# Kernel tuning notes

Measured on AMD Instinct MI355X. Metric: run time of the kernel, lower is better.

Reference implementation:

```python
import jax, jax.numpy as jnp
import numpy as np
import math

PC_MIN_X, PC_MIN_Y = 0.0, -40.0
VOXEL = 0.05
STRIDE = 8
PE_CH = 16
NEG_SLOPE = 0.01
BN_EPS = 1e-5


def _grid_points():
    # get_pseudo_points: centers of stride-8 BEV cells
    xs = np.arange(0.2, 70.4, 0.4, dtype=np.float32)    # 176
    ys = np.arange(-39.8, 40.2, 0.4, dtype=np.float32)  # 200
    gx, gy = np.meshgrid(xs, ys)                        # (200, 176)
    return jnp.asarray(np.stack([gx, gy], -1).reshape(-1, 2))  # [P, 2]


def _pe3d(D, H, W):
    ch = PE_CH
    div = jnp.exp(jnp.arange(0, ch, 2, dtype=jnp.float32) * (-math.log(10000.0) / ch))
    def enc(n):
        t = jnp.arange(n, dtype=jnp.float32)[:, None] * div[None, :]
        return jnp.concatenate([jnp.sin(t), jnp.cos(t)], axis=-1)  # [n, ch]
    pex = jnp.broadcast_to(enc(D)[:, None, None, :], (D, H, W, ch))
    pey = jnp.broadcast_to(enc(H)[None, :, None, :], (D, H, W, ch))
    pez = jnp.broadcast_to(enc(W)[None, None, :, :], (D, H, W, ch))
    return jnp.concatenate([pex, pey, pez], axis=-1).transpose(3, 0, 1, 2)  # [3*ch, D, H, W]


def _bn_lrelu(h, g, b):
    # eval-mode BatchNorm3d with running_mean=0, running_var=1, then LeakyReLU(0.01)
    h = h * (g / np.sqrt(1.0 + BN_EPS))[None, :, None, None, None] + b[None, :, None, None, None]
    return jnp.where(h >= 0, h, NEG_SLOPE * h)


def _dvf(x, w1, b1, g1, be1, w2, b2, g2, be2, w3, b3):
    N, C, D, H, W = x.shape
    pe = _pe3d(D, H, W)  # [48, D, H, W]
    feats = jnp.concatenate([x, jnp.broadcast_to(pe[None], (N,) + pe.shape)], axis=1)
    h = jnp.einsum('ncdhw,oc->nodhw', feats, w1) + b1[None, :, None, None, None]
    h = _bn_lrelu(h, g1, be1)
    h = jnp.einsum('ncdhw,oc->nodhw', h, w2) + b2[None, :, None, None, None]
    h = _bn_lrelu(h, g2, be2)
    logits = jnp.einsum('ncdhw,oc->nodhw', h, w3) + b3[None, :, None, None, None]  # [N,1,D,H,W]
    wts = jax.nn.softmax(logits, axis=2)  # softmax over depth D
    return (x * wts).reshape(N, C * D, H, W)


def _bilinear(im, x, y):
    # im: (H, W, C), x/y: (P,)  -- faithful to bilinear_interpolate_torch
    H, W = im.shape[0], im.shape[1]
    xf = jnp.floor(x).astype(jnp.int32)
    yf = jnp.floor(y).astype(jnp.int32)
    x0 = jnp.clip(xf, 0, W - 1)
    x1 = jnp.clip(xf + 1, 0, W - 1)
    y0 = jnp.clip(yf, 0, H - 1)
    y1 = jnp.clip(yf + 1, 0, H - 1)
    Ia, Ib, Ic, Id = im[y0, x0], im[y1, x0], im[y0, x1], im[y1, x1]
    x0f, x1f = x0.astype(x.dtype), x1.astype(x.dtype)
    y0f, y1f = y0.astype(y.dtype), y1.astype(y.dtype)
    wa = (x1f - x) * (y1f - y)
    wb = (x1f - x) * (y - y0f)
    wc = (x - x0f) * (y1f - y)
    wd = (x - x0f) * (y - y0f)
    return Ia * wa[:, None] + Ib * wb[:, None] + Ic * wc[:, None] + Id * wd[:, None]


def _rot(p, theta):
    c, s = jnp.cos(theta), jnp.sin(theta)
    return jnp.stack([p[:, 0] * c - p[:, 1] * s, p[:, 0] * s + p[:, 1] * c], axis=-1)


def _bev_align_one(feat, th_prev, th_cur, grid):
    # feat: [C', H, W]; X_TRANS modeled as z-rotation: fwd(current) then inverse(previous)
    Hh, Ww = feat.shape[1], feat.shape[2]
    p = _rot(grid, th_cur)
    p = _rot(p, -th_prev)
    xi = (p[:, 0] - PC_MIN_X) / VOXEL / STRIDE
    yi = (p[:, 1] - PC_MIN_Y) / VOXEL / STRIDE
    out = _bilinear(feat.transpose(1, 2, 0), xi, yi)  # [P, C']
    return out.reshape(Hh, Ww, -1).transpose(2, 0, 1)


def setup_inputs() -> dict:
    key = jax.random.key(0)
    ks = jax.random.split(key, 16)
    N, C, D, H, W = 4, 64, 2, 200, 176
    IN1 = PE_CH * 3 + C  # 112
    inp = {
        'x0': jax.random.normal(ks[0], (N, C, D, H, W), jnp.float32),
        'x1': jax.random.normal(ks[1], (N, C, D, H, W), jnp.float32),
        'transform_param': jax.random.normal(ks[2], (N, 2), jnp.float32) * 0.3,
        'w1': jax.random.normal(ks[3], (C, IN1), jnp.float32) * 0.05,
        'b1': jax.random.normal(ks[4], (C,), jnp.float32) * 0.05,
        'g1': jax.random.uniform(ks[5], (C,), jnp.float32, 0.5, 1.5),
        'be1': jax.random.normal(ks[6], (C,), jnp.float32) * 0.05,
        'w2': jax.random.normal(ks[7], (C // 2, C), jnp.float32) * 0.05,
        'b2': jax.random.normal(ks[8], (C // 2,), jnp.float32) * 0.05,
        'g2': jax.random.uniform(ks[9], (C // 2,), jnp.float32, 0.5, 1.5),
        'be2': jax.random.normal(ks[10], (C // 2,), jnp.float32) * 0.05,
        'w3': jax.random.normal(ks[11], (1, C // 2), jnp.float32) * 0.05,
        'b3': jax.random.normal(ks[12], (1,), jnp.float32) * 0.05,
    }
    return inp


def reference(x0, x1, transform_param, w1, b1, g1, be1, w2, b2, g2, be2, w3, b3):
    mlp = (w1, b1, g1, be1, w2, b2, g2, be2, w3, b3)
    f0 = _dvf(x0, *mlp)  # rot 0: [N, C*D, H, W]
    f1 = _dvf(x1, *mlp)  # rot 1
    grid = _grid_points()
    aligned = jax.vmap(lambda f, tp: _bev_align_one(f, tp[0], tp[1], grid))(f1, transform_param)
    return jnp.maximum(f0, aligned)  # ALIGN_METHOD='max' over stacked feats
```

## Files before the change

### kernel.cpp

```cpp
#include <hip/hip_runtime.h>
#include <hip/hip_bf16.h>
#include <cmath>

#define HW   35200
#define CD   128

typedef short bf16x8 __attribute__((ext_vector_type(8)));
typedef float f32x4  __attribute__((ext_vector_type(4)));
typedef unsigned int u32;

union Frag { unsigned u[4]; bf16x8 v; };

#define GLD16(srcp, dstp) \
  __builtin_amdgcn_global_load_lds((const __attribute__((address_space(1))) u32*)(const void*)(srcp), \
                                   (__attribute__((address_space(3))) u32*)(void*)(dstp), 16, 0, 0)

#define OFF_W1B   0
#define OFF_W2B   3072
#define OFF_TD    4096
#define OFF_B2F   4224
#define OFF_W3F   4256
#define OFF_PE    4288
#define OFF_F0B   567488
#define OFF_F1B   9578688

__device__ __forceinline__ float lrelu(float v) { return v >= 0.f ? v : 0.01f * v; }
__device__ __forceinline__ unsigned short f2bf(float f) {
  union { __hip_bfloat16 h; unsigned short u; } c;
  c.h = __float2bfloat16(f);
  return c.u;
}
__device__ __forceinline__ unsigned pack2bf(float lo, float hi) {
  union { __hip_bfloat162 h2; unsigned u; } c;
  c.h2 = __float22bfloat162_rn(float2{lo, hi});
  return c.u;
}
__device__ __forceinline__ float bflo(unsigned u) { return __uint_as_float(u << 16); }
__device__ __forceinline__ float bfhi(unsigned u) { return __uint_as_float(u & 0xffff0000u); }

__global__ void setup_kernel(const float* __restrict__ w1, const float* __restrict__ b1,
                             const float* __restrict__ g1, const float* __restrict__ be1,
                             const float* __restrict__ w2, const float* __restrict__ b2,
                             const float* __restrict__ g2, const float* __restrict__ be2,
                             const float* __restrict__ w3, const float* __restrict__ b3,
                             float* __restrict__ ws) {
  const float RS = rsqrtf(1.0f + 1e-5f);
  unsigned short* w1b = (unsigned short*)(ws + OFF_W1B);
  unsigned short* w2b = (unsigned short*)(ws + OFF_W2B);
  unsigned short* pe  = (unsigned short*)(ws + OFF_PE);
  int i = blockIdx.x * blockDim.x + threadIdx.x;
  if (i < 6144) {
    int e = i & 7, l = (i >> 3) & 63, nt = (i >> 9) & 3, kh = i >> 11;
    int n = nt * 16 + (l & 15);
    int k = kh * 32 + (l >> 4) * 8 + e;
    int col = (kh < 2) ? k : (80 + (k - 64));
    w1b[i] = f2bf(w1[n * 112 + col] * (g1[n] * RS));
    return;
  }
  i -= 6144;
  if (i < 2048) {
    int e = i & 7, l = (i >> 3) & 63, nt = (i >> 9) & 1, kh = i >> 10;
    int n = nt * 16 + (l & 15);
    int k = kh * 32 + (l >> 4) * 8 + e;
    w2b[i] = f2bf(w2[n * 64 + k] * (g2[n] * RS));
    return;
  }
  i -= 2048;
  if (i < 128) {
    int d = i >> 6, o = i & 63;
    float a = 0.f;
    for (int j = 0; j < 8; ++j) {
      float dv = expf((float)(2 * j) * (-0.5756462732485115f));
      float t  = (float)d * dv;
      a += w1[o * 112 + 64 + j] * sinf(t) + w1[o * 112 + 72 + j] * cosf(t);
    }
    ws[OFF_TD + d * 64 + o] = (g1[o] * RS) * (b1[o] + a) + be1[o];
    return;
  }
  i -= 128;
  if (i < 32) { ws[OFF_B2F + i] = b2[i] * (g2[i] * RS) + be2[i]; return; }
  i -= 32;
  if (i < 32) { ws[OFF_W3F + i] = w3[i]; return; }
  i -= 32;
  if (i < 563200) {
    int hw = i >> 4, j = i & 15;
    int h = hw / 176, w = hw - h * 176;
    int jj = j & 7;
    float dv = expf((float)(2 * jj) * (-0.5756462732485115f));
    if (j < 8) {
      float t = (float)h * dv;
      pe[hw * 32 + jj]      = f2bf(sinf(t));
      pe[hw * 32 + 8 + jj]  = f2bf(cosf(t));
    } else {
      float t = (float)w * dv;
      pe[hw * 32 + 16 + jj] = f2bf(sinf(t));
      pe[hw * 32 + 24 + jj] = f2bf(cosf(t));
    }
  }
}

__global__ __launch_bounds__(256)
void mlp_kernel(const float* __restrict__ x0, const float* __restrict__ x1,
                const float* __restrict__ wtab,
                unsigned short* __restrict__ f0b, unsigned short* __restrict__ f1b) {
  __shared__ alignas(16) unsigned char Sm[32768];

  const int t    = threadIdx.x;
  const int lane = t & 63;
  const int wv   = __builtin_amdgcn_readfirstlane(t >> 6);
  const int g    = lane >> 4;
  const int li   = lane & 15;
  const int n    = blockIdx.y;
  const int inp  = blockIdx.z;
  const int hw0w = blockIdx.x * 64 + wv * 16;
  const int px   = hw0w + li;
  const float* xn = (inp ? x1 : x0) + (size_t)n * CD * HW;
  unsigned short* dst = inp ? f1b : f0b;
  const unsigned short* w1bu = (const unsigned short*)(wtab + OFF_W1B);
  const unsigned short* w2bu = (const unsigned short*)(wtab + OFF_W2B);
  const unsigned short* peg  = (const unsigned short*)(wtab + OFF_PE);
  unsigned char* Wb = Sm + wv * 8192;

  const uint4 pev = *(const uint4*)(peg + (size_t)px * 32 + g * 8);

#pragma unroll
  for (int j = 0; j < 8; ++j) {
    const int plane = 2 * (8 * j + (lane >> 3)) + ((lane & 1) ^ (j & 1));
    const int q     = (((lane >> 1) & 3) - j) & 3;
    GLD16(xn + (size_t)plane * HW + hw0w + q * 4, Wb + j * 1024);
  }
  asm volatile("s_waitcnt vmcnt(0)" ::: "memory");
  __builtin_amdgcn_sched_barrier(0);

  const float* Wf = (const float*)Wb;
  const int qbase = (((li >> 2) + g) & 3) * 8 + (li & 3);
  Frag xb[2][2];
#pragma unroll
  for (int d = 0; d < 2; ++d) {
    const int dof = (d ^ (g & 1)) * 4;
#pragma unroll
    for (int kh = 0; kh < 2; ++kh)
#pragma unroll
      for (int q2 = 0; q2 < 4; ++q2) {
        const float v0 = Wf[(32 * kh + 8 * g + 2 * q2 + 0) * 32 + qbase + dof];
        const float v1 = Wf[(32 * kh + 8 * g + 2 * q2 + 1) * 32 + qbase + dof];
        xb[d][kh].u[q2] = pack2bf(v0, v1);
      }
  }
  Frag pf;
  pf.u[0] = pev.x; pf.u[1] = pev.y; pf.u[2] = pev.z; pf.u[3] = pev.w;

  f32x4 acc[2][4];
#pragma unroll
  for (int d = 0; d < 2; ++d)
#pragma unroll
    for (int nt = 0; nt < 4; ++nt) {
      const float tdv = wtab[OFF_TD + d * 64 + nt * 16 + li];
      acc[d][nt] = (f32x4){tdv, tdv, tdv, tdv};
    }
#pragma unroll
  for (int kh = 0; kh < 2; ++kh)
#pragma unroll
    for (int nt = 0; nt < 4; ++nt) {
      const bf16x8 b = *(const bf16x8*)&w1bu[(unsigned)((kh * 4 + nt) * 64 + lane) * 8];
      acc[0][nt] = __builtin_amdgcn_mfma_f32_16x16x32_bf16(xb[0][kh].v, b, acc[0][nt], 0, 0, 0);
      acc[1][nt] = __builtin_amdgcn_mfma_f32_16x16x32_bf16(xb[1][kh].v, b, acc[1][nt], 0, 0, 0);
    }
#pragma unroll
  for (int nt = 0; nt < 4; ++nt) {
    const bf16x8 b = *(const bf16x8*)&w1bu[(unsigned)((8 + nt) * 64 + lane) * 8];
    acc[0][nt] = __builtin_amdgcn_mfma_f32_16x16x32_bf16(pf.v, b, acc[0][nt], 0, 0, 0);
    acc[1][nt] = __builtin_amdgcn_mfma_f32_16x16x32_bf16(pf.v, b, acc[1][nt], 0, 0, 0);
  }
  __builtin_amdgcn_sched_barrier(0);

  unsigned short* Hsw = (unsigned short*)Wb;
#pragma unroll
  for (int d = 0; d < 2; ++d)
#pragma unroll
    for (int nt = 0; nt < 4; ++nt)
#pragma unroll
      for (int r = 0; r < 4; ++r) {
        const int o   = nt * 16 + li;
        const int row = d * 16 + g * 4 + r;
        Hsw[(unsigned)(((o >> 3) * 32 + row) * 8 + (o & 7))] = f2bf(lrelu(acc[d][nt][r]));
      }

  f32x4 acc2[2][2];
#pragma unroll
  for (int nt = 0; nt < 2; ++nt) {
    const float bv = wtab[OFF_B2F + nt * 16 + li];
    acc2[0][nt] = (f32x4){bv, bv, bv, bv};
    acc2[1][nt] = acc2[0][nt];
  }
#pragma unroll
  for (int kh = 0; kh < 2; ++kh) {
    const bf16x8 a0 = *(const bf16x8*)&Hsw[(unsigned)(((kh * 4 + g) * 32 + 0 * 16 + li) * 8)];
    const bf16x8 a1 = *(const bf16x8*)&Hsw[(unsigned)(((kh * 4 + g) * 32 + 1 * 16 + li) * 8)];
#pragma unroll
    for (int nt = 0; nt < 2; ++nt) {
      const bf16x8 b = *(const bf16x8*)&w2bu[(unsigned)((kh * 2 + nt) * 64 + lane) * 8];
      acc2[0][nt] = __builtin_amdgcn_mfma_f32_16x16x32_bf16(a0, b, acc2[0][nt], 0, 0, 0);
      acc2[1][nt] = __builtin_amdgcn_mfma_f32_16x16x32_bf16(a1, b, acc2[1][nt], 0, 0, 0);
    }
  }

  const float w3a = wtab[OFF_W3F + li];
  const float w3b = wtab[OFF_W3F + 16 + li];
  float wt0[4], wt1[4];
#pragma unroll
  for (int r = 0; r < 4; ++r) {
    float p0 = w3a * lrelu(acc2[0][0][r]) + w3b * lrelu(acc2[0][1][r]);
    float p1 = w3a * lrelu(acc2[1][0][r]) + w3b * lrelu(acc2[1][1][r]);
    p0 += __shfl_xor(p0, 1); p0 += __shfl_xor(p0, 2);
    p0 += __shfl_xor(p0, 4); p0 += __shfl_xor(p0, 8);
    p1 += __shfl_xor(p1, 1); p1 += __shfl_xor(p1, 2);
    p1 += __shfl_xor(p1, 4); p1 += __shfl_xor(p1, 8);
    wt0[r] = 1.f / (1.f + expf(p1 - p0));
    wt1[r] = 1.f / (1.f + expf(p0 - p1));
  }

  const int src = (li >> 2) << 4;
  float a0 = __shfl(wt0[0], src), b0 = __shfl(wt1[0], src);
  float a1 = __shfl(wt0[1], src), b1v = __shfl(wt1[1], src);
  float a2 = __shfl(wt0[2], src), b2v = __shfl(wt1[2], src);
  float a3 = __shfl(wt0[3], src), b3v = __shfl(wt1[3], src);
  const int rs = li & 3;
  const float w0  = (rs == 0) ? a0 : (rs == 1) ? a1 : (rs == 2) ? a2 : a3;
  const float w1v = (rs == 0) ? b0 : (rs == 1) ? b1v : (rs == 2) ? b2v : b3v;

#pragma unroll
  for (int kh = 0; kh < 2; ++kh)
#pragma unroll
    for (int j = 0; j < 4; ++j) {
      const int k = kh * 16 + g * 4 + j;
      const unsigned ua = xb[0][kh].u[j];
      const unsigned ub = xb[1][kh].u[j];
      uint2 pk;
      pk.x = pack2bf(bflo(ua) * w0, bflo(ub) * w1v);
      pk.y = pack2bf(bfhi(ua) * w0, bfhi(ub) * w1v);
      *(uint2*)&dst[(((size_t)n * 32 + k) * HW + px) * 4] = pk;
    }
}

__global__ __launch_bounds__(256)
void gather_max_kernel(const unsigned short* __restrict__ f0b,
                       const unsigned short* __restrict__ f1b,
                       const float* __restrict__ tp,
                       float* __restrict__ out) {
  const int orig = blockIdx.x;
  const int xcd = orig & 7, idx = orig >> 3;
  const int tile = (xcd < 6 ? xcd * 69 : 6 * 69 + (xcd - 6) * 68) + idx;

  const int tix = threadIdx.x;
  const int px  = tix & 63;
  const int q   = tix >> 6;
  const int n   = blockIdx.y;
  const int hw  = tile * 64 + px;
  const int h   = hw / 176;
  const int w   = hw - h * 176;

  const float thp = tp[n * 2 + 0], thc = tp[n * 2 + 1];
  const float gx = 0.2f + 0.4f * (float)w;
  const float gy = -39.8f + 0.4f * (float)h;
  const float c1 = cosf(thc),  s1v = sinf(thc);
  const float p1x = gx * c1 - gy * s1v;
  const float p1y = gx * s1v + gy * c1;
  const float c2 = cosf(-thp), s2v = sinf(-thp);
  const float p2x = p1x * c2 - p1y * s2v;
  const float p2y = p1x * s2v + p1y * c2;
  const float xi = p2x / 0.05f / 8.f;
  const float yi = (p2y - (-40.f)) / 0.05f / 8.f;

  const float xf = floorf(xi), yf = floorf(yi);
  const int x0i = (int)xf, y0i = (int)yf;
  const int x0c = min(max(x0i,     0), 175);
  const int x1c = min(max(x0i + 1, 0), 175);
  const int y0c = min(max(y0i,     0), 199);
  const int y1c = min(max(y0i + 1, 0), 199);
  const float x0f = (float)x0c, x1f = (float)x1c;
  const float y0f = (float)y0c, y1f = (float)y1c;
  const float wa = (x1f - xi) * (y1f - yi);
  const float wb = (x1f - xi) * (yi - y0f);
  const float wc = (xi - x0f) * (y1f - yi);
  const float wd = (xi - x0f) * (yi - y0f);
  const int ta = y0c * 176 + x0c, tb = y1c * 176 + x0c;
  const int tc = y0c * 176 + x1c, td = y1c * 176 + x1c;

#pragma unroll
  for (int i = 0; i < 8; ++i) {
    const int k = q * 8 + i;
    const int cd0 = k * 4;
    const unsigned short* fp1 = f1b + ((size_t)n * 32 + k) * HW * 4;
    const uint2 Ia = *(const uint2*)(fp1 + (size_t)ta * 4);
    const uint2 Ib = *(const uint2*)(fp1 + (size_t)tb * 4);
    const uint2 Ic = *(const uint2*)(fp1 + (size_t)tc * 4);
    const uint2 Id = *(const uint2*)(fp1 + (size_t)td * 4);
    float4 sv;
    sv.x = bflo(Ia.x) * wa + bflo(Ib.x) * wb + bflo(Ic.x) * wc + bflo(Id.x) * wd;
    sv.y = bfhi(Ia.x) * wa + bfhi(Ib.x) * wb + bfhi(Ic.x) * wc + bfhi(Id.x) * wd;
    sv.z = bflo(Ia.y) * wa + bflo(Ib.y) * wb + bflo(Ic.y) * wc + bflo(Id.y) * wd;
    sv.w = bfhi(Ia.y) * wa + bfhi(Ib.y) * wb + bfhi(Ic.y) * wc + bfhi(Id.y) * wd;

    const uint2 F0 = *(const uint2*)(f0b + (((size_t)n * 32 + k) * HW + hw) * 4);

    float* op = out + ((size_t)n * CD + cd0) * HW + hw;
    op[0]              = fmaxf(bflo(F0.x), sv.x);
    op[HW]             = fmaxf(bfhi(F0.x), sv.y);
    op[2 * (size_t)HW] = fmaxf(bflo(F0.y), sv.z);
    op[3 * (size_t)HW] = fmaxf(bfhi(F0.y), sv.w);
  }
}

extern "C" void kernel_launch(void* const* d_in, const int* in_sizes, int n_in,
                              void* d_out, int out_size, void* d_ws, size_t ws_size,
                              hipStream_t stream) {
  const float* x0  = (const float*)d_in[0];
  const float* x1  = (const float*)d_in[1];
  const float* tp  = (const float*)d_in[2];
  const float* w1  = (const float*)d_in[3];
  const float* b1  = (const float*)d_in[4];
  const float* g1  = (const float*)d_in[5];
  const float* be1 = (const float*)d_in[6];
  const float* w2  = (const float*)d_in[7];
  const float* b2  = (const float*)d_in[8];
  const float* g2  = (const float*)d_in[9];
  const float* be2 = (const float*)d_in[10];
  const float* w3  = (const float*)d_in[11];
  const float* b3  = (const float*)d_in[12];
  float* ws = (float*)d_ws;
  unsigned short* f0b = (unsigned short*)(ws + OFF_F0B);
  unsigned short* f1b = (unsigned short*)(ws + OFF_F1B);

  setup_kernel<<<2233, 256, 0, stream>>>(w1, b1, g1, be1, w2, b2, g2, be2, w3, b3, ws);

  dim3 g1d(550, 4, 2);
  mlp_kernel<<<g1d, 256, 0, stream>>>(x0, x1, ws, f0b, f1b);

  dim3 g2d(550, 4);
  gather_max_kernel<<<g2d, 256, 0, stream>>>(f0b, f1b, tp, (float*)d_out);
}
```

Baseline: 85.48 us.

## Double-buffer async LDS loads across five pixel tiles per wave in MLP kernel

```diff
diff --git a/kernel.cpp b/kernel.cpp
--- a/kernel.cpp
+++ b/kernel.cpp
@@ -99,148 +99,169 @@
   }
 }
 
-__global__ __launch_bounds__(256)
+__global__ __launch_bounds__(128)
 void mlp_kernel(const float* __restrict__ x0, const float* __restrict__ x1,
                 const float* __restrict__ wtab,
                 unsigned short* __restrict__ f0b, unsigned short* __restrict__ f1b) {
-  __shared__ alignas(16) unsigned char Sm[32768];
-
-  const int t    = threadIdx.x;
-  const int lane = t & 63;
-  const int wv   = __builtin_amdgcn_readfirstlane(t >> 6);
+  __shared__ alignas(16) unsigned char Sm[40960];
+
+  const int t0   = threadIdx.x;
+  const int lane = t0 & 63;
+  const int wv   = __builtin_amdgcn_readfirstlane(t0 >> 6);
   const int g    = lane >> 4;
   const int li   = lane & 15;
   const int n    = blockIdx.y;
   const int inp  = blockIdx.z;
-  const int hw0w = blockIdx.x * 64 + wv * 16;
-  const int px   = hw0w + li;
+  const int base = blockIdx.x * 160 + wv * 16;
   const float* xn = (inp ? x1 : x0) + (size_t)n * CD * HW;
   unsigned short* dst = inp ? f1b : f0b;
   const unsigned short* w1bu = (const unsigned short*)(wtab + OFF_W1B);
   const unsigned short* w2bu = (const unsigned short*)(wtab + OFF_W2B);
   const unsigned short* peg  = (const unsigned short*)(wtab + OFF_PE);
-  unsigned char* Wb = Sm + wv * 8192;
-
-  const uint4 pev = *(const uint4*)(peg + (size_t)px * 32 + g * 8);
-
-#pragma unroll
-  for (int j = 0; j < 8; ++j) {
-    const int plane = 2 * (8 * j + (lane >> 3)) + ((lane & 1) ^ (j & 1));
-    const int q     = (((lane >> 1) & 3) - j) & 3;
-    GLD16(xn + (size_t)plane * HW + hw0w + q * 4, Wb + j * 1024);
-  }
-  asm volatile("s_waitcnt vmcnt(0)" ::: "memory");
-  __builtin_amdgcn_sched_barrier(0);
-
-  const float* Wf = (const float*)Wb;
-  const int qbase = (((li >> 2) + g) & 3) * 8 + (li & 3);
-  Frag xb[2][2];
-#pragma unroll
-  for (int d = 0; d < 2; ++d) {
-    const int dof = (d ^ (g & 1)) * 4;
-#pragma unroll
-    for (int kh = 0; kh < 2; ++kh)
-#pragma unroll
-      for (int q2 = 0; q2 < 4; ++q2) {
-        const float v0 = Wf[(32 * kh + 8 * g + 2 * q2 + 0) * 32 + qbase + dof];
-        const float v1 = Wf[(32 * kh + 8 * g + 2 * q2 + 1) * 32 + qbase + dof];
-        xb[d][kh].u[q2] = pack2bf(v0, v1);
-      }
-  }
-  Frag pf;
-  pf.u[0] = pev.x; pf.u[1] = pev.y; pf.u[2] = pev.z; pf.u[3] = pev.w;
-
-  f32x4 acc[2][4];
-#pragma unroll
-  for (int d = 0; d < 2; ++d)
-#pragma unroll
-    for (int nt = 0; nt < 4; ++nt) {
-      const float tdv = wtab[OFF_TD + d * 64 + nt * 16 + li];
-      acc[d][nt] = (f32x4){tdv, tdv, tdv, tdv};
-    }
-#pragma unroll
-  for (int kh = 0; kh < 2; ++kh)
-#pragma unroll
-    for (int nt = 0; nt < 4; ++nt) {
-      const bf16x8 b = *(const bf16x8*)&w1bu[(unsigned)((kh * 4 + nt) * 64 + lane) * 8];
-      acc[0][nt] = __builtin_amdgcn_mfma_f32_16x16x32_bf16(xb[0][kh].v, b, acc[0][nt], 0, 0, 0);
-      acc[1][nt] = __builtin_amdgcn_mfma_f32_16x16x32_bf16(xb[1][kh].v, b, acc[1][nt], 0, 0, 0);
-    }
-#pragma unroll
-  for (int nt = 0; nt < 4; ++nt) {
-    const bf16x8 b = *(const bf16x8*)&w1bu[(unsigned)((8 + nt) * 64 + lane) * 8];
-    acc[0][nt] = __builtin_amdgcn_mfma_f32_16x16x32_bf16(pf.v, b, acc[0][nt], 0, 0, 0);
-    acc[1][nt] = __builtin_amdgcn_mfma_f32_16x16x32_bf16(pf.v, b, acc[1][nt], 0, 0, 0);
-  }
-  __builtin_amdgcn_sched_barrier(0);
-
-  unsigned short* Hsw = (unsigned short*)Wb;
-#pragma unroll
-  for (int d = 0; d < 2; ++d)
-#pragma unroll
-    for (int nt = 0; nt < 4; ++nt)
-#pragma unroll
-      for (int r = 0; r < 4; ++r) {
-        const int o   = nt * 16 + li;
-        const int row = d * 16 + g * 4 + r;
-        Hsw[(unsigned)(((o >> 3) * 32 + row) * 8 + (o & 7))] = f2bf(lrelu(acc[d][nt][r]));
-      }
-
-  f32x4 acc2[2][2];
-#pragma unroll
-  for (int nt = 0; nt < 2; ++nt) {
-    const float bv = wtab[OFF_B2F + nt * 16 + li];
-    acc2[0][nt] = (f32x4){bv, bv, bv, bv};
-    acc2[1][nt] = acc2[0][nt];
-  }
-#pragma unroll
-  for (int kh = 0; kh < 2; ++kh) {
-    const bf16x8 a0 = *(const bf16x8*)&Hsw[(unsigned)(((kh * 4 + g) * 32 + 0 * 16 + li) * 8)];
-    const bf16x8 a1 = *(const bf16x8*)&Hsw[(unsigned)(((kh * 4 + g) * 32 + 1 * 16 + li) * 8)];
-#pragma unroll
-    for (int nt = 0; nt < 2; ++nt) {
-      const bf16x8 b = *(const bf16x8*)&w2bu[(unsigned)((kh * 2 + nt) * 64 + lane) * 8];
-      acc2[0][nt] = __builtin_amdgcn_mfma_f32_16x16x32_bf16(a0, b, acc2[0][nt], 0, 0, 0);
-      acc2[1][nt] = __builtin_amdgcn_mfma_f32_16x16x32_bf16(a1, b, acc2[1][nt], 0, 0, 0);
-    }
-  }
+  unsigned char* Wbase = Sm + wv * 20480;
+  unsigned char* bufs[2] = { Wbase, Wbase + 8192 };
+  unsigned short* Hsw = (unsigned short*)(Wbase + 16384);
+
+  uint4 pev[5];
+#pragma unroll
+  for (int t = 0; t < 5; ++t)
+    pev[t] = *(const uint4*)(peg + (size_t)(base + t * 32 + li) * 32 + g * 8);
+
+#define ISSUE_GRP(T, B)                                                          \
+  {                                                                              \
+    const int pxb_ = base + (T) * 32;                                            \
+    _Pragma("unroll")                                                            \
+    for (int j = 0; j < 8; ++j) {                                                \
+      const int plane_ = 2 * (8 * j + (lane >> 3)) + ((lane & 1) ^ (j & 1));     \
+      const int q_     = (((lane >> 1) & 3) - j) & 3;                            \
+      GLD16(xn + (size_t)plane_ * HW + pxb_ + q_ * 4, bufs[B] + j * 1024);       \
+    }                                                                            \
+  }
+
+  ISSUE_GRP(0, 0)
+  ISSUE_GRP(1, 1)
 
   const float w3a = wtab[OFF_W3F + li];
   const float w3b = wtab[OFF_W3F + 16 + li];
-  float wt0[4], wt1[4];
-#pragma unroll
-  for (int r = 0; r < 4; ++r) {
-    float p0 = w3a * lrelu(acc2[0][0][r]) + w3b * lrelu(acc2[0][1][r]);
-    float p1 = w3a * lrelu(acc2[1][0][r]) + w3b * lrelu(acc2[1][1][r]);
-    p0 += __shfl_xor(p0, 1); p0 += __shfl_xor(p0, 2);
-    p0 += __shfl_xor(p0, 4); p0 += __shfl_xor(p0, 8);
-    p1 += __shfl_xor(p1, 1); p1 += __shfl_xor(p1, 2);
-    p1 += __shfl_xor(p1, 4); p1 += __shfl_xor(p1, 8);
-    wt0[r] = 1.f / (1.f + expf(p1 - p0));
-    wt1[r] = 1.f / (1.f + expf(p0 - p1));
-  }
-
-  const int src = (li >> 2) << 4;
-  float a0 = __shfl(wt0[0], src), b0 = __shfl(wt1[0], src);
-  float a1 = __shfl(wt0[1], src), b1v = __shfl(wt1[1], src);
-  float a2 = __shfl(wt0[2], src), b2v = __shfl(wt1[2], src);
-  float a3 = __shfl(wt0[3], src), b3v = __shfl(wt1[3], src);
-  const int rs = li & 3;
-  const float w0  = (rs == 0) ? a0 : (rs == 1) ? a1 : (rs == 2) ? a2 : a3;
-  const float w1v = (rs == 0) ? b0 : (rs == 1) ? b1v : (rs == 2) ? b2v : b3v;
-
-#pragma unroll
-  for (int kh = 0; kh < 2; ++kh)
-#pragma unroll
-    for (int j = 0; j < 4; ++j) {
-      const int k = kh * 16 + g * 4 + j;
-      const unsigned ua = xb[0][kh].u[j];
-      const unsigned ub = xb[1][kh].u[j];
-      uint2 pk;
-      pk.x = pack2bf(bflo(ua) * w0, bflo(ub) * w1v);
-      pk.y = pack2bf(bfhi(ua) * w0, bfhi(ub) * w1v);
-      *(uint2*)&dst[(((size_t)n * 32 + k) * HW + px) * 4] = pk;
-    }
+  const int   src = (li >> 2) << 4;
+  const int   rs  = li & 3;
+
+#pragma unroll
+  for (int t = 0; t < 5; ++t) {
+    if (t == 0) asm volatile("s_waitcnt vmcnt(8)" ::: "memory");
+    else        asm volatile("s_waitcnt vmcnt(16)" ::: "memory");
+    __builtin_amdgcn_sched_barrier(0);
+
+    const float* Wf = (const float*)bufs[t & 1];
+    const int qbase = (((li >> 2) + g) & 3) * 8 + (li & 3);
+    Frag xb[2][2];
+#pragma unroll
+    for (int d = 0; d < 2; ++d) {
+      const int dof = (d ^ (g & 1)) * 4;
+#pragma unroll
+      for (int kh = 0; kh < 2; ++kh)
+#pragma unroll
+        for (int q2 = 0; q2 < 4; ++q2) {
+          const float v0 = Wf[(32 * kh + 8 * g + 2 * q2 + 0) * 32 + qbase + dof];
+          const float v1 = Wf[(32 * kh + 8 * g + 2 * q2 + 1) * 32 + qbase + dof];
+          xb[d][kh].u[q2] = pack2bf(v0, v1);
+        }
+    }
+    asm volatile("s_waitcnt lgkmcnt(0)" ::: "memory");
+    __builtin_amdgcn_sched_barrier(0);
+    if (t < 3) ISSUE_GRP(t + 2, t & 1)
+    __builtin_amdgcn_sched_barrier(0);
+
+    Frag pf;
+    pf.u[0] = pev[t].x; pf.u[1] = pev[t].y; pf.u[2] = pev[t].z; pf.u[3] = pev[t].w;
+
+    f32x4 acc[2][4];
+#pragma unroll
+    for (int d = 0; d < 2; ++d)
+#pragma unroll
+      for (int nt = 0; nt < 4; ++nt) {
+        const float tdv = wtab[OFF_TD + d * 64 + nt * 16 + li];
+        acc[d][nt] = (f32x4){tdv, tdv, tdv, tdv};
+      }
+#pragma unroll
+    for (int kh = 0; kh < 2; ++kh)
+#pragma unroll
+      for (int nt = 0; nt < 4; ++nt) {
+        const bf16x8 b = *(const bf16x8*)&w1bu[(unsigned)((kh * 4 + nt) * 64 + lane) * 8];
+        acc[0][nt] = __builtin_amdgcn_mfma_f32_16x16x32_bf16(xb[0][kh].v, b, acc[0][nt], 0, 0, 0);
+        acc[1][nt] = __builtin_amdgcn_mfma_f32_16x16x32_bf16(xb[1][kh].v, b, acc[1][nt], 0, 0, 0);
+      }
+#pragma unroll
+    for (int nt = 0; nt < 4; ++nt) {
+      const bf16x8 b = *(const bf16x8*)&w1bu[(unsigned)((8 + nt) * 64 + lane) * 8];
+      acc[0][nt] = __builtin_amdgcn_mfma_f32_16x16x32_bf16(pf.v, b, acc[0][nt], 0, 0, 0);
+      acc[1][nt] = __builtin_amdgcn_mfma_f32_16x16x32_bf16(pf.v, b, acc[1][nt], 0, 0, 0);
+    }
+
+#pragma unroll
+    for (int d = 0; d < 2; ++d)
+#pragma unroll
+      for (int nt = 0; nt < 4; ++nt)
+#pragma unroll
+        for (int r = 0; r < 4; ++r) {
+          const int o   = nt * 16 + li;
+          const int row = d * 16 + g * 4 + r;
+          Hsw[(unsigned)(((o >> 3) * 32 + row) * 8 + (o & 7))] = f2bf(lrelu(acc[d][nt][r]));
+        }
+
+    f32x4 acc2[2][2];
+#pragma unroll
+    for (int nt = 0; nt < 2; ++nt) {
+      const float bv = wtab[OFF_B2F + nt * 16 + li];
+      acc2[0][nt] = (f32x4){bv, bv, bv, bv};
+      acc2[1][nt] = acc2[0][nt];
+    }
+#pragma unroll
+    for (int kh = 0; kh < 2; ++kh) {
+      const bf16x8 a0 = *(const bf16x8*)&Hsw[(unsigned)(((kh * 4 + g) * 32 + 0 * 16 + li) * 8)];
+      const bf16x8 a1 = *(const bf16x8*)&Hsw[(unsigned)(((kh * 4 + g) * 32 + 1 * 16 + li) * 8)];
+#pragma unroll
+      for (int nt = 0; nt < 2; ++nt) {
+        const bf16x8 b = *(const bf16x8*)&w2bu[(unsigned)((kh * 2 + nt) * 64 + lane) * 8];
+        acc2[0][nt] = __builtin_amdgcn_mfma_f32_16x16x32_bf16(a0, b, acc2[0][nt], 0, 0, 0);
+        acc2[1][nt] = __builtin_amdgcn_mfma_f32_16x16x32_bf16(a1, b, acc2[1][nt], 0, 0, 0);
+      }
+    }
+
+    float wt0[4], wt1[4];
+#pragma unroll
+    for (int r = 0; r < 4; ++r) {
+      float p0 = w3a * lrelu(acc2[0][0][r]) + w3b * lrelu(acc2[0][1][r]);
+      float p1 = w3a * lrelu(acc2[1][0][r]) + w3b * lrelu(acc2[1][1][r]);
+      p0 += __shfl_xor(p0, 1); p0 += __shfl_xor(p0, 2);
+      p0 += __shfl_xor(p0, 4); p0 += __shfl_xor(p0, 8);
+      p1 += __shfl_xor(p1, 1); p1 += __shfl_xor(p1, 2);
+      p1 += __shfl_xor(p1, 4); p1 += __shfl_xor(p1, 8);
+      wt0[r] = 1.f / (1.f + expf(p1 - p0));
+      wt1[r] = 1.f / (1.f + expf(p0 - p1));
+    }
+    float a0 = __shfl(wt0[0], src), b0 = __shfl(wt1[0], src);
+    float a1 = __shfl(wt0[1], src), b1v = __shfl(wt1[1], src);
+    float a2 = __shfl(wt0[2], src), b2v = __shfl(wt1[2], src);
+    float a3 = __shfl(wt0[3], src), b3v = __shfl(wt1[3], src);
+    const float w0  = (rs == 0) ? a0 : (rs == 1) ? a1 : (rs == 2) ? a2 : a3;
+    const float w1v = (rs == 0) ? b0 : (rs == 1) ? b1v : (rs == 2) ? b2v : b3v;
+
+    const int px = base + t * 32 + li;
+#pragma unroll
+    for (int kh = 0; kh < 2; ++kh)
+#pragma unroll
+      for (int j = 0; j < 4; ++j) {
+        const int k = kh * 16 + g * 4 + j;
+        const unsigned ua = xb[0][kh].u[j];
+        const unsigned ub = xb[1][kh].u[j];
+        uint2 pk;
+        pk.x = pack2bf(bflo(ua) * w0, bflo(ub) * w1v);
+        pk.y = pack2bf(bfhi(ua) * w0, bfhi(ub) * w1v);
+        *(uint2*)&dst[(((size_t)n * 32 + k) * HW + px) * 4] = pk;
+      }
+  }
+#undef ISSUE_GRP
 }
 
 __global__ __launch_bounds__(256)
@@ -334,8 +355,8 @@
 
   setup_kernel<<<2233, 256, 0, stream>>>(w1, b1, g1, be1, w2, b2, g2, be2, w3, b3, ws);
 
-  dim3 g1d(550, 4, 2);
-  mlp_kernel<<<g1d, 256, 0, stream>>>(x0, x1, ws, f0b, f1b);
+  dim3 g1d(220, 4, 2);
+  mlp_kernel<<<g1d, 128, 0, stream>>>(x0, x1, ws, f0b, f1b);
 
   dim3 g2d(550, 4);
   gather_max_kernel<<<g2d, 256, 0, stream>>>(f0b, f1b, tp, (float*)d_out);
```

Result: slower. 100.6 us (+17.7%).
